# Performance work log

Measured on AMD Instinct MI355X. Metric: run time of the kernel, lower is better.

## Reference

```python
import math
import jax, jax.numpy as jnp
import numpy as np

B, Q, K, D = 32, 1024, 1024, 128
MASK_VALUE = -1000000.0


def setup_inputs() -> dict:
    key = jax.random.key(0)
    kq, kk, kv, kl = jax.random.split(key, 4)
    return {
        "queries": jax.random.normal(kq, (B, Q, D), dtype=jnp.float32),
        "keys": jax.random.normal(kk, (B, K, D), dtype=jnp.float32),
        "values": jax.random.normal(kv, (B, K, D), dtype=jnp.float32),
        "valid_lens": jax.random.randint(kl, (B,), 1, K + 1, dtype=jnp.int32),
    }


def reference(queries, keys, values, valid_lens):
    d = queries.shape[-1]
    # scores: [B, Q, K]
    scores = jnp.einsum("bqd,bkd->bqk", queries, keys) / math.sqrt(d)
    # key-padding mask: position k valid iff k < valid_lens[b] (broadcast over queries)
    mask = jnp.arange(keys.shape[1])[None, None, :] < valid_lens[:, None, None]
    scores = jnp.where(mask, scores, MASK_VALUE)
    attn = jax.nn.softmax(scores, axis=-1)
    # dropout p=0.0 -> identity
    return jnp.einsum("bqk,bkv->bqv", attn, values)
```

## Files before the change

kernel.cpp:

```cpp
#include <hip/hip_runtime.h>
#include <math.h>

typedef _Float16 f16;
typedef __attribute__((ext_vector_type(8))) _Float16 f16x8;
typedef __attribute__((ext_vector_type(4))) _Float16 f16x4;
typedef __attribute__((ext_vector_type(4))) float f32x4;

constexpr int BATCH = 32;
constexpr int QL = 1024;
constexpr int KL = 1024;
constexpr int D = 128;
constexpr int BQ = 64;
constexpr int BK = 64;
constexpr int DKP = 136;
constexpr int BKP = 72;

#define CSC 0.12752863187087177f

__global__ __launch_bounds__(256, 2)
void attn_fwd(const float* __restrict__ Qp, const float* __restrict__ Kp,
              const float* __restrict__ Vp, const int* __restrict__ VLp,
              float* __restrict__ Op) {
  __shared__ f16 sK[2][BK][DKP];
  __shared__ f16 sVT[2][D][BKP];
  __shared__ f16 sP[4][16][BKP];

  const int tid  = threadIdx.x;
  const int wave = tid >> 6, lane = tid & 63;
  const int l16  = lane & 15, quad = lane >> 4;

  const int id = blockIdx.x;
  const int b  = (((id >> 3) & 3) << 3) | (id & 7);
  const int qt = id >> 5;
  const int vl = VLp[b];

  const float* Kb = Kp + (size_t)b * KL * D;
  const float* Vb = Vp + (size_t)b * KL * D;
  const int ntiles = (vl + BK - 1) / BK;

  const int kf_row[8] = {
    (tid + 0*256) >> 5, (tid + 1*256) >> 5, (tid + 2*256) >> 5, (tid + 3*256) >> 5,
    (tid + 4*256) >> 5, (tid + 5*256) >> 5, (tid + 6*256) >> 5, (tid + 7*256) >> 5 };
  const int kf_c4 = tid & 31;

  float4 kreg[8], vreg[8];

  {
    const float4* Kt = (const float4*)Kb;
    #pragma unroll
    for (int i = 0; i < 8; ++i) kreg[i] = Kt[tid + i * 256];
    #pragma unroll
    for (int i = 0; i < 2; ++i) {
      int f = tid + i * 256;
      const float* base = Vb + (size_t)((f & 15) * 4) * D + (f >> 4) * 4;
      vreg[i * 4 + 0] = *(const float4*)(base);
      vreg[i * 4 + 1] = *(const float4*)(base + D);
      vreg[i * 4 + 2] = *(const float4*)(base + 2 * D);
      vreg[i * 4 + 3] = *(const float4*)(base + 3 * D);
    }
  }

  const float* Qb = Qp + ((size_t)(b * QL + qt * BQ + wave * 16 + l16)) * D;
  f16x8 qfrag[4];
  #pragma unroll
  for (int kc = 0; kc < 4; ++kc) {
    const float* p = Qb + kc * 32 + quad * 8;
    float4 u = *(const float4*)p;
    float4 v = *(const float4*)(p + 4);
    f16x8 f;
    f[0] = (f16)u.x; f[1] = (f16)u.y; f[2] = (f16)u.z; f[3] = (f16)u.w;
    f[4] = (f16)v.x; f[5] = (f16)v.y; f[6] = (f16)v.z; f[7] = (f16)v.w;
    qfrag[kc] = f;
  }

  float m2[4]   = {-INFINITY, -INFINITY, -INFINITY, -INFINITY};
  float lsum[4] = {0.f, 0.f, 0.f, 0.f};
  f32x4 o[8];
  #pragma unroll
  for (int dt = 0; dt < 8; ++dt) o[dt] = (f32x4){0.f, 0.f, 0.f, 0.f};

  #pragma unroll
  for (int i = 0; i < 8; ++i) {
    int row = kf_row[i];
    int rp = (row & 3) * 16 + (row >> 2);
    float4 u = kreg[i];
    f16x4 h;
    h[0] = (f16)u.x; h[1] = (f16)u.y; h[2] = (f16)u.z; h[3] = (f16)u.w;
    *(f16x4*)&sK[0][rp][kf_c4 * 4] = h;
  }
  #pragma unroll
  for (int i = 0; i < 2; ++i) {
    int f = tid + i * 256;
    int k0 = (f & 15) * 4, d0 = (f >> 4) * 4;
    float4 r0 = vreg[i * 4 + 0], r1 = vreg[i * 4 + 1];
    float4 r2 = vreg[i * 4 + 2], r3 = vreg[i * 4 + 3];
    f16x4 h;
    h[0] = (f16)r0.x; h[1] = (f16)r1.x; h[2] = (f16)r2.x; h[3] = (f16)r3.x;
    *(f16x4*)&sVT[0][d0 + 0][k0] = h;
    h[0] = (f16)r0.y; h[1] = (f16)r1.y; h[2] = (f16)r2.y; h[3] = (f16)r3.y;
    *(f16x4*)&sVT[0][d0 + 1][k0] = h;
    h[0] = (f16)r0.z; h[1] = (f16)r1.z; h[2] = (f16)r2.z; h[3] = (f16)r3.z;
    *(f16x4*)&sVT[0][d0 + 2][k0] = h;
    h[0] = (f16)r0.w; h[1] = (f16)r1.w; h[2] = (f16)r2.w; h[3] = (f16)r3.w;
    *(f16x4*)&sVT[0][d0 + 3][k0] = h;
  }
  __syncthreads();

  for (int t = 0; t < ntiles; ++t) {
    const int cur = t & 1, nxt = cur ^ 1;
    const bool more = (t + 1 < ntiles);

    if (more) {
      const float4* Kt = (const float4*)(Kb + (size_t)(t + 1) * BK * D);
      #pragma unroll
      for (int i = 0; i < 8; ++i) kreg[i] = Kt[tid + i * 256];
      const float* Vt = Vb + (size_t)(t + 1) * BK * D;
      #pragma unroll
      for (int i = 0; i < 2; ++i) {
        int f = tid + i * 256;
        const float* base = Vt + (size_t)((f & 15) * 4) * D + (f >> 4) * 4;
        vreg[i * 4 + 0] = *(const float4*)(base);
        vreg[i * 4 + 1] = *(const float4*)(base + D);
        vreg[i * 4 + 2] = *(const float4*)(base + 2 * D);
        vreg[i * 4 + 3] = *(const float4*)(base + 3 * D);
      }
    }

    f32x4 s[4];
    #pragma unroll
    for (int ct = 0; ct < 4; ++ct) {
      f32x4 c = (f32x4){0.f, 0.f, 0.f, 0.f};
      #pragma unroll
      for (int kc = 0; kc < 4; ++kc) {
        f16x8 kf = *(const f16x8*)&sK[cur][ct * 16 + l16][kc * 32 + quad * 8];
        c = __builtin_amdgcn_mfma_f32_16x16x32_f16(qfrag[kc], kf, c, 0, 0, 0);
      }
      s[ct] = c;
    }

    #pragma unroll
    for (int ct = 0; ct < 4; ++ct) {
      bool ok = (t * BK + l16 * 4 + ct) < vl;
      #pragma unroll
      for (int r = 0; r < 4; ++r)
        s[ct][r] = ok ? s[ct][r] * CSC : -1.0e9f;
    }

    float mnew[4], alpha[4], ls[4];
    #pragma unroll
    for (int r = 0; r < 4; ++r) {
      float v = fmaxf(fmaxf(s[0][r], s[1][r]), fmaxf(s[2][r], s[3][r]));
      v = fmaxf(v, __shfl_xor(v, 1));
      v = fmaxf(v, __shfl_xor(v, 2));
      v = fmaxf(v, __shfl_xor(v, 4));
      v = fmaxf(v, __shfl_xor(v, 8));
      mnew[r]  = fmaxf(m2[r], v);
      alpha[r] = __builtin_amdgcn_exp2f(m2[r] - mnew[r]);
      m2[r]    = mnew[r];
      ls[r]    = 0.f;
    }
    #pragma unroll
    for (int ct = 0; ct < 4; ++ct)
      #pragma unroll
      for (int r = 0; r < 4; ++r) {
        float p = __builtin_amdgcn_exp2f(s[ct][r] - mnew[r]);
        s[ct][r] = p;
        ls[r] += p;
      }
    #pragma unroll
    for (int r = 0; r < 4; ++r) {
      float v = ls[r];
      v += __shfl_xor(v, 1);
      v += __shfl_xor(v, 2);
      v += __shfl_xor(v, 4);
      v += __shfl_xor(v, 8);
      lsum[r] = lsum[r] * alpha[r] + v;
    }

    #pragma unroll
    for (int r = 0; r < 4; ++r) {
      f16x4 h;
      h[0] = (f16)s[0][r]; h[1] = (f16)s[1][r];
      h[2] = (f16)s[2][r]; h[3] = (f16)s[3][r];
      *(f16x4*)&sP[wave][quad * 4 + r][l16 * 4] = h;
    }
    #pragma unroll
    for (int dt = 0; dt < 8; ++dt)
      #pragma unroll
      for (int r = 0; r < 4; ++r)
        o[dt][r] *= alpha[r];

    asm volatile("s_waitcnt lgkmcnt(0)" ::: "memory");

    #pragma unroll
    for (int ks = 0; ks < 2; ++ks) {
      f16x8 pf = *(const f16x8*)&sP[wave][l16][ks * 32 + quad * 8];
      #pragma unroll
      for (int dt = 0; dt < 8; ++dt) {
        f16x8 vf = *(const f16x8*)&sVT[cur][dt * 16 + l16][ks * 32 + quad * 8];
        o[dt] = __builtin_amdgcn_mfma_f32_16x16x32_f16(pf, vf, o[dt], 0, 0, 0);
      }
    }

    if (more) {
      #pragma unroll
      for (int i = 0; i < 8; ++i) {
        int row = kf_row[i];
        int rp = (row & 3) * 16 + (row >> 2);
        float4 u = kreg[i];
        f16x4 h;
        h[0] = (f16)u.x; h[1] = (f16)u.y; h[2] = (f16)u.z; h[3] = (f16)u.w;
        *(f16x4*)&sK[nxt][rp][kf_c4 * 4] = h;
      }
      #pragma unroll
      for (int i = 0; i < 2; ++i) {
        int f = tid + i * 256;
        int k0 = (f & 15) * 4, d0 = (f >> 4) * 4;
        float4 r0 = vreg[i * 4 + 0], r1 = vreg[i * 4 + 1];
        float4 r2 = vreg[i * 4 + 2], r3 = vreg[i * 4 + 3];
        f16x4 h;
        h[0] = (f16)r0.x; h[1] = (f16)r1.x; h[2] = (f16)r2.x; h[3] = (f16)r3.x;
        *(f16x4*)&sVT[nxt][d0 + 0][k0] = h;
        h[0] = (f16)r0.y; h[1] = (f16)r1.y; h[2] = (f16)r2.y; h[3] = (f16)r3.y;
        *(f16x4*)&sVT[nxt][d0 + 1][k0] = h;
        h[0] = (f16)r0.z; h[1] = (f16)r1.z; h[2] = (f16)r2.z; h[3] = (f16)r3.z;
        *(f16x4*)&sVT[nxt][d0 + 2][k0] = h;
        h[0] = (f16)r0.w; h[1] = (f16)r1.w; h[2] = (f16)r2.w; h[3] = (f16)r3.w;
        *(f16x4*)&sVT[nxt][d0 + 3][k0] = h;
      }
    }
    __syncthreads();
  }

  float* Ob = Op + ((size_t)(b * QL + qt * BQ + wave * 16)) * D;
  #pragma unroll
  for (int r = 0; r < 4; ++r) {
    float inv = 1.0f / lsum[r];
    int row = quad * 4 + r;
    #pragma unroll
    for (int dt = 0; dt < 8; ++dt)
      Ob[(size_t)row * D + dt * 16 + l16] = o[dt][r] * inv;
  }
}

extern "C" void kernel_launch(void* const* d_in, const int* in_sizes, int n_in,
                              void* d_out, int out_size, void* d_ws, size_t ws_size,
                              hipStream_t stream) {
  const float* Qp = (const float*)d_in[0];
  const float* Kp = (const float*)d_in[1];
  const float* Vp = (const float*)d_in[2];
  const int*   VL = (const int*)d_in[3];
  float* Op = (float*)d_out;

  attn_fwd<<<dim3(QL / BQ * BATCH), dim3(256), 0, stream>>>(Qp, Kp, Vp, VL, Op);
}
```

Measured before the change: 130.0 us.

## Double query tile per block with two MFMA row tiles per wave

Raises the query block from 64 to 128 rows, so each wave computes two 16-row tiles against every staged K/V tile. Each K/V tile is then loaded, converted to fp16 and written to shared memory half as often per query row. Launch bounds move to one block per CU, and the grid shrinks to 256 blocks, which lowers occupancy and may worsen load balance across batches with different valid lengths. Float-to-half conversions now use packed round-toward-zero instructions instead of per-element casts, which slightly changes rounding.

```diff
diff --git a/kernel.cpp b/kernel.cpp
--- a/kernel.cpp
+++ b/kernel.cpp
@@ -10,20 +10,28 @@
 constexpr int QL = 1024;
 constexpr int KL = 1024;
 constexpr int D = 128;
-constexpr int BQ = 64;
+constexpr int BQ = 128;
 constexpr int BK = 64;
 constexpr int DKP = 136;
 constexpr int BKP = 72;
 
 #define CSC 0.12752863187087177f
 
-__global__ __launch_bounds__(256, 2)
+static __device__ __forceinline__ f16x4 pk4(float x, float y, float z, float w) {
+  auto a = __builtin_amdgcn_cvt_pkrtz(x, y);
+  auto b = __builtin_amdgcn_cvt_pkrtz(z, w);
+  f16x4 h;
+  h[0] = (f16)a[0]; h[1] = (f16)a[1]; h[2] = (f16)b[0]; h[3] = (f16)b[1];
+  return h;
+}
+
+__global__ __launch_bounds__(256, 1)
 void attn_fwd(const float* __restrict__ Qp, const float* __restrict__ Kp,
               const float* __restrict__ Vp, const int* __restrict__ VLp,
               float* __restrict__ Op) {
   __shared__ f16 sK[2][BK][DKP];
   __shared__ f16 sVT[2][D][BKP];
-  __shared__ f16 sP[4][16][BKP];
+  __shared__ f16 sP[4][32][BKP];
 
   const int tid  = threadIdx.x;
   const int wave = tid >> 6, lane = tid & 63;
@@ -37,11 +45,6 @@
   const float* Kb = Kp + (size_t)b * KL * D;
   const float* Vb = Vp + (size_t)b * KL * D;
   const int ntiles = (vl + BK - 1) / BK;
-
-  const int kf_row[8] = {
-    (tid + 0*256) >> 5, (tid + 1*256) >> 5, (tid + 2*256) >> 5, (tid + 3*256) >> 5,
-    (tid + 4*256) >> 5, (tid + 5*256) >> 5, (tid + 6*256) >> 5, (tid + 7*256) >> 5 };
-  const int kf_c4 = tid & 31;
 
   float4 kreg[8], vreg[8];
 
@@ -60,49 +63,52 @@
     }
   }
 
-  const float* Qb = Qp + ((size_t)(b * QL + qt * BQ + wave * 16 + l16)) * D;
-  f16x8 qfrag[4];
-  #pragma unroll
-  for (int kc = 0; kc < 4; ++kc) {
-    const float* p = Qb + kc * 32 + quad * 8;
-    float4 u = *(const float4*)p;
-    float4 v = *(const float4*)(p + 4);
-    f16x8 f;
-    f[0] = (f16)u.x; f[1] = (f16)u.y; f[2] = (f16)u.z; f[3] = (f16)u.w;
-    f[4] = (f16)v.x; f[5] = (f16)v.y; f[6] = (f16)v.z; f[7] = (f16)v.w;
-    qfrag[kc] = f;
-  }
-
-  float m2[4]   = {-INFINITY, -INFINITY, -INFINITY, -INFINITY};
-  float lsum[4] = {0.f, 0.f, 0.f, 0.f};
-  f32x4 o[8];
-  #pragma unroll
-  for (int dt = 0; dt < 8; ++dt) o[dt] = (f32x4){0.f, 0.f, 0.f, 0.f};
+  f16x8 qfrag[2][4];
+  #pragma unroll
+  for (int mt = 0; mt < 2; ++mt) {
+    const float* Qb =
+        Qp + ((size_t)(b * QL + qt * BQ + wave * 32 + mt * 16 + l16)) * D;
+    #pragma unroll
+    for (int kc = 0; kc < 4; ++kc) {
+      const float* p = Qb + kc * 32 + quad * 8;
+      float4 u = *(const float4*)p;
+      float4 v = *(const float4*)(p + 4);
+      f16x4 h0 = pk4(u.x, u.y, u.z, u.w);
+      f16x4 h1 = pk4(v.x, v.y, v.z, v.w);
+      f16x8 f;
+      f[0] = h0[0]; f[1] = h0[1]; f[2] = h0[2]; f[3] = h0[3];
+      f[4] = h1[0]; f[5] = h1[1]; f[6] = h1[2]; f[7] = h1[3];
+      qfrag[mt][kc] = f;
+    }
+  }
+
+  float m2[2][4], lsum[2][4];
+  f32x4 o[2][8];
+  #pragma unroll
+  for (int mt = 0; mt < 2; ++mt)
+    #pragma unroll
+    for (int r = 0; r < 4; ++r) { m2[mt][r] = -INFINITY; lsum[mt][r] = 0.f; }
+  #pragma unroll
+  for (int mt = 0; mt < 2; ++mt)
+    #pragma unroll
+    for (int dt = 0; dt < 8; ++dt) o[mt][dt] = (f32x4){0.f, 0.f, 0.f, 0.f};
 
   #pragma unroll
   for (int i = 0; i < 8; ++i) {
-    int row = kf_row[i];
+    int row = (tid + i * 256) >> 5;
     int rp = (row & 3) * 16 + (row >> 2);
     float4 u = kreg[i];
-    f16x4 h;
-    h[0] = (f16)u.x; h[1] = (f16)u.y; h[2] = (f16)u.z; h[3] = (f16)u.w;
-    *(f16x4*)&sK[0][rp][kf_c4 * 4] = h;
+    *(f16x4*)&sK[0][rp][(tid & 31) * 4] = pk4(u.x, u.y, u.z, u.w);
   }
   #pragma unroll
   for (int i = 0; i < 2; ++i) {
     int f = tid + i * 256;
     int k0 = (f & 15) * 4, d0 = (f >> 4) * 4;
-    float4 r0 = vreg[i * 4 + 0], r1 = vreg[i * 4 + 1];
-    float4 r2 = vreg[i * 4 + 2], r3 = vreg[i * 4 + 3];
-    f16x4 h;
-    h[0] = (f16)r0.x; h[1] = (f16)r1.x; h[2] = (f16)r2.x; h[3] = (f16)r3.x;
-    *(f16x4*)&sVT[0][d0 + 0][k0] = h;
-    h[0] = (f16)r0.y; h[1] = (f16)r1.y; h[2] = (f16)r2.y; h[3] = (f16)r3.y;
-    *(f16x4*)&sVT[0][d0 + 1][k0] = h;
-    h[0] = (f16)r0.z; h[1] = (f16)r1.z; h[2] = (f16)r2.z; h[3] = (f16)r3.z;
-    *(f16x4*)&sVT[0][d0 + 2][k0] = h;
-    h[0] = (f16)r0.w; h[1] = (f16)r1.w; h[2] = (f16)r2.w; h[3] = (f16)r3.w;
-    *(f16x4*)&sVT[0][d0 + 3][k0] = h;
+    float4 r0 = vreg[i*4+0], r1 = vreg[i*4+1], r2 = vreg[i*4+2], r3 = vreg[i*4+3];
+    *(f16x4*)&sVT[0][d0 + 0][k0] = pk4(r0.x, r1.x, r2.x, r3.x);
+    *(f16x4*)&sVT[0][d0 + 1][k0] = pk4(r0.y, r1.y, r2.y, r3.y);
+    *(f16x4*)&sVT[0][d0 + 2][k0] = pk4(r0.z, r1.z, r2.z, r3.z);
+    *(f16x4*)&sVT[0][d0 + 3][k0] = pk4(r0.w, r1.w, r2.w, r3.w);
   }
   __syncthreads();
 
@@ -126,121 +132,117 @@
       }
     }
 
-    f32x4 s[4];
+    f32x4 s[2][4];
     #pragma unroll
     for (int ct = 0; ct < 4; ++ct) {
-      f32x4 c = (f32x4){0.f, 0.f, 0.f, 0.f};
+      f32x4 c0 = (f32x4){0.f, 0.f, 0.f, 0.f};
+      f32x4 c1 = (f32x4){0.f, 0.f, 0.f, 0.f};
       #pragma unroll
       for (int kc = 0; kc < 4; ++kc) {
         f16x8 kf = *(const f16x8*)&sK[cur][ct * 16 + l16][kc * 32 + quad * 8];
-        c = __builtin_amdgcn_mfma_f32_16x16x32_f16(qfrag[kc], kf, c, 0, 0, 0);
-      }
-      s[ct] = c;
+        c0 = __builtin_amdgcn_mfma_f32_16x16x32_f16(qfrag[0][kc], kf, c0, 0, 0, 0);
+        c1 = __builtin_amdgcn_mfma_f32_16x16x32_f16(qfrag[1][kc], kf, c1, 0, 0, 0);
+      }
+      s[0][ct] = c0;
+      s[1][ct] = c1;
     }
 
     #pragma unroll
     for (int ct = 0; ct < 4; ++ct) {
       bool ok = (t * BK + l16 * 4 + ct) < vl;
       #pragma unroll
-      for (int r = 0; r < 4; ++r)
-        s[ct][r] = ok ? s[ct][r] * CSC : -1.0e9f;
-    }
-
-    float mnew[4], alpha[4], ls[4];
-    #pragma unroll
-    for (int r = 0; r < 4; ++r) {
-      float v = fmaxf(fmaxf(s[0][r], s[1][r]), fmaxf(s[2][r], s[3][r]));
-      v = fmaxf(v, __shfl_xor(v, 1));
-      v = fmaxf(v, __shfl_xor(v, 2));
-      v = fmaxf(v, __shfl_xor(v, 4));
-      v = fmaxf(v, __shfl_xor(v, 8));
-      mnew[r]  = fmaxf(m2[r], v);
-      alpha[r] = __builtin_amdgcn_exp2f(m2[r] - mnew[r]);
-      m2[r]    = mnew[r];
-      ls[r]    = 0.f;
-    }
-    #pragma unroll
-    for (int ct = 0; ct < 4; ++ct)
+      for (int mt = 0; mt < 2; ++mt)
+        #pragma unroll
+        for (int r = 0; r < 4; ++r)
+          s[mt][ct][r] = ok ? s[mt][ct][r] * CSC : -1.0e9f;
+    }
+
+    #pragma unroll
+    for (int mt = 0; mt < 2; ++mt) {
+      float mnew[4], alpha[4], ls[4];
       #pragma unroll
       for (int r = 0; r < 4; ++r) {
-        float p = __builtin_amdgcn_exp2f(s[ct][r] - mnew[r]);
-        s[ct][r] = p;
-        ls[r] += p;
-      }
-    #pragma unroll
-    for (int r = 0; r < 4; ++r) {
-      float v = ls[r];
-      v += __shfl_xor(v, 1);
-      v += __shfl_xor(v, 2);
-      v += __shfl_xor(v, 4);
-      v += __shfl_xor(v, 8);
-      lsum[r] = lsum[r] * alpha[r] + v;
-    }
-
-    #pragma unroll
-    for (int r = 0; r < 4; ++r) {
-      f16x4 h;
-      h[0] = (f16)s[0][r]; h[1] = (f16)s[1][r];
-      h[2] = (f16)s[2][r]; h[3] = (f16)s[3][r];
-      *(f16x4*)&sP[wave][quad * 4 + r][l16 * 4] = h;
-    }
-    #pragma unroll
-    for (int dt = 0; dt < 8; ++dt)
-      #pragma unroll
-      for (int r = 0; r < 4; ++r)
-        o[dt][r] *= alpha[r];
+        float v = fmaxf(fmaxf(s[mt][0][r], s[mt][1][r]),
+                        fmaxf(s[mt][2][r], s[mt][3][r]));
+        v = fmaxf(v, __shfl_xor(v, 1));
+        v = fmaxf(v, __shfl_xor(v, 2));
+        v = fmaxf(v, __shfl_xor(v, 4));
+        v = fmaxf(v, __shfl_xor(v, 8));
+        mnew[r]  = fmaxf(m2[mt][r], v);
+        alpha[r] = __builtin_amdgcn_exp2f(m2[mt][r] - mnew[r]);
+        m2[mt][r] = mnew[r];
+        ls[r] = 0.f;
+      }
+      #pragma unroll
+      for (int ct = 0; ct < 4; ++ct)
+        #pragma unroll
+        for (int r = 0; r < 4; ++r) {
+          float p = __builtin_amdgcn_exp2f(s[mt][ct][r] - mnew[r]);
+          s[mt][ct][r] = p;
+          ls[r] += p;
+        }
+      #pragma unroll
+      for (int r = 0; r < 4; ++r) {
+        float v = ls[r];
+        v += __shfl_xor(v, 1);
+        v += __shfl_xor(v, 2);
+        v += __shfl_xor(v, 4);
+        v += __shfl_xor(v, 8);
+        lsum[mt][r] = lsum[mt][r] * alpha[r] + v;
+        *(f16x4*)&sP[wave][mt * 16 + quad * 4 + r][l16 * 4] =
+            pk4(s[mt][0][r], s[mt][1][r], s[mt][2][r], s[mt][3][r]);
+        #pragma unroll
+        for (int dt = 0; dt < 8; ++dt) o[mt][dt][r] *= alpha[r];
+      }
+    }
 
     asm volatile("s_waitcnt lgkmcnt(0)" ::: "memory");
 
     #pragma unroll
     for (int ks = 0; ks < 2; ++ks) {
-      f16x8 pf = *(const f16x8*)&sP[wave][l16][ks * 32 + quad * 8];
+      f16x8 pf0 = *(const f16x8*)&sP[wave][l16][ks * 32 + quad * 8];
+      f16x8 pf1 = *(const f16x8*)&sP[wave][16 + l16][ks * 32 + quad * 8];
       #pragma unroll
       for (int dt = 0; dt < 8; ++dt) {
         f16x8 vf = *(const f16x8*)&sVT[cur][dt * 16 + l16][ks * 32 + quad * 8];
-        o[dt] = __builtin_amdgcn_mfma_f32_16x16x32_f16(pf, vf, o[dt], 0, 0, 0);
+        o[0][dt] = __builtin_amdgcn_mfma_f32_16x16x32_f16(pf0, vf, o[0][dt], 0, 0, 0);
+        o[1][dt] = __builtin_amdgcn_mfma_f32_16x16x32_f16(pf1, vf, o[1][dt], 0, 0, 0);
       }
     }
 
     if (more) {
       #pragma unroll
       for (int i = 0; i < 8; ++i) {
-        int row = kf_row[i];
+        int row = (tid + i * 256) >> 5;
         int rp = (row & 3) * 16 + (row >> 2);
         float4 u = kreg[i];
-        f16x4 h;
-        h[0] = (f16)u.x; h[1] = (f16)u.y; h[2] = (f16)u.z; h[3] = (f16)u.w;
-        *(f16x4*)&sK[nxt][rp][kf_c4 * 4] = h;
+        *(f16x4*)&sK[nxt][rp][(tid & 31) * 4] = pk4(u.x, u.y, u.z, u.w);
       }
       #pragma unroll
       for (int i = 0; i < 2; ++i) {
         int f = tid + i * 256;
         int k0 = (f & 15) * 4, d0 = (f >> 4) * 4;
-        float4 r0 = vreg[i * 4 + 0], r1 = vreg[i * 4 + 1];
-        float4 r2 = vreg[i * 4 + 2], r3 = vreg[i * 4 + 3];
-        f16x4 h;
-        h[0] = (f16)r0.x; h[1] = (f16)r1.x; h[2] = (f16)r2.x; h[3] = (f16)r3.x;
-        *(f16x4*)&sVT[nxt][d0 + 0][k0] = h;
-        h[0] = (f16)r0.y; h[1] = (f16)r1.y; h[2] = (f16)r2.y; h[3] = (f16)r3.y;
-        *(f16x4*)&sVT[nxt][d0 + 1][k0] = h;
-        h[0] = (f16)r0.z; h[1] = (f16)r1.z; h[2] = (f16)r2.z; h[3] = (f16)r3.z;
-        *(f16x4*)&sVT[nxt][d0 + 2][k0] = h;
-        h[0] = (f16)r0.w; h[1] = (f16)r1.w; h[2] = (f16)r2.w; h[3] = (f16)r3.w;
-        *(f16x4*)&sVT[nxt][d0 + 3][k0] = h;
+        float4 r0 = vreg[i*4+0], r1 = vreg[i*4+1], r2 = vreg[i*4+2], r3 = vreg[i*4+3];
+        *(f16x4*)&sVT[nxt][d0 + 0][k0] = pk4(r0.x, r1.x, r2.x, r3.x);
+        *(f16x4*)&sVT[nxt][d0 + 1][k0] = pk4(r0.y, r1.y, r2.y, r3.y);
+        *(f16x4*)&sVT[nxt][d0 + 2][k0] = pk4(r0.z, r1.z, r2.z, r3.z);
+        *(f16x4*)&sVT[nxt][d0 + 3][k0] = pk4(r0.w, r1.w, r2.w, r3.w);
       }
     }
     __syncthreads();
   }
 
-  float* Ob = Op + ((size_t)(b * QL + qt * BQ + wave * 16)) * D;
-  #pragma unroll
-  for (int r = 0; r < 4; ++r) {
-    float inv = 1.0f / lsum[r];
-    int row = quad * 4 + r;
-    #pragma unroll
-    for (int dt = 0; dt < 8; ++dt)
-      Ob[(size_t)row * D + dt * 16 + l16] = o[dt][r] * inv;
-  }
+  float* Ob = Op + ((size_t)(b * QL + qt * BQ + wave * 32)) * D;
+  #pragma unroll
+  for (int mt = 0; mt < 2; ++mt)
+    #pragma unroll
+    for (int r = 0; r < 4; ++r) {
+      float inv = 1.0f / lsum[mt][r];
+      int row = mt * 16 + quad * 4 + r;
+      #pragma unroll
+      for (int dt = 0; dt < 8; ++dt)
+        Ob[(size_t)row * D + dt * 16 + l16] = o[mt][dt][r] * inv;
+    }
 }
 
 extern "C" void kernel_launch(void* const* d_in, const int* in_sizes, int n_in,
```

New measurement: 146.0 us. +12.4%, slower.
